# Performance work log

Hardware: AMD Instinct MI355X
Metric: run time of the kernel (lower is better)

## Reference

```python
import jax, jax.numpy as jnp
import numpy as np

H = 256       # hidden_dim
DICT = 30     # dict_size
SOS = 1       # symb2int['<sos>']

def gru_cell(x, h, Wih, Whh, bih, bhh):
    # PyTorch GRU cell math
    gi = x @ Wih.T + bih
    gh = h @ Whh.T + bhh
    ir, iz, inn = jnp.split(gi, 3, axis=-1)
    hr, hz, hn = jnp.split(gh, 3, axis=-1)
    r = jax.nn.sigmoid(ir + hr)
    z = jax.nn.sigmoid(iz + hz)
    n = jnp.tanh(inn + r * hn)
    return (1.0 - z) * n + z * h

def run_gru(xs, h0, Wih, Whh, bih, bhh):
    # xs: [T, B, F] -> outputs [T, B, Hc], final hidden [B, Hc]
    def step(h, x):
        h = gru_cell(x, h, Wih, Whh, bih, bhh)
        return h, h
    hT, out = jax.lax.scan(step, h0, xs)
    return out, hT

def setup_inputs() -> dict:
    key = jax.random.key(0)
    ks = jax.random.split(key, 24)
    B, T, L = 128, 512, 64
    se = 1.0 / np.sqrt(H)        # encoder GRU init scale
    sd = 1.0 / np.sqrt(2 * H)    # decoder GRU / linears scale
    def r(k, shape, sc):
        return jax.random.normal(k, shape, jnp.float32) * sc
    return {
        "x": jax.random.normal(ks[0], (B, T, 2), jnp.float32),
        "target_seq": jax.random.randint(ks[1], (B, L), 0, DICT),
        # encoder GRU, forward direction
        "enc_Wih_f": r(ks[2], (3 * H, 2), se), "enc_Whh_f": r(ks[3], (3 * H, H), se),
        "enc_bih_f": r(ks[4], (3 * H,), se),   "enc_bhh_f": r(ks[5], (3 * H,), se),
        # encoder GRU, backward direction
        "enc_Wih_b": r(ks[6], (3 * H, 2), se), "enc_Whh_b": r(ks[7], (3 * H, H), se),
        "enc_bih_b": r(ks[8], (3 * H,), se),   "enc_bhh_b": r(ks[9], (3 * H,), se),
        # decoder embedding + GRU (hidden 2H)
        "emb": r(ks[10], (DICT, H), 1.0),
        "dec_Wih": r(ks[11], (6 * H, H), sd),     "dec_Whh": r(ks[12], (6 * H, 2 * H), sd),
        "dec_bih": r(ks[13], (6 * H,), sd),       "dec_bhh": r(ks[14], (6 * H,), sd),
        # hidden2query, att_combine, fc
        "Wq": r(ks[15], (2 * H, 2 * H), sd), "bq": r(ks[16], (2 * H,), sd),
        "Wc": r(ks[17], (H, 4 * H), sd),     "bc": r(ks[18], (H,), sd),
        "Wf": r(ks[19], (DICT, H), se),      "bf": r(ks[20], (DICT,), se),
    }

def reference(x, target_seq,
              enc_Wih_f, enc_Whh_f, enc_bih_f, enc_bhh_f,
              enc_Wih_b, enc_Whh_b, enc_bih_b, enc_bhh_b,
              emb, dec_Wih, dec_Whh, dec_bih, dec_bhh,
              Wq, bq, Wc, bc, Wf, bf):
    B = x.shape[0]
    xs = jnp.transpose(x, (1, 0, 2))                # [T, B, 2]
    h0 = jnp.zeros((B, H), x.dtype)
    out_f, hf = run_gru(xs, h0, enc_Wih_f, enc_Whh_f, enc_bih_f, enc_bhh_f)
    out_b, hb = run_gru(xs[::-1], h0, enc_Wih_b, enc_Whh_b, enc_bih_b, enc_bhh_b)
    enc_out = jnp.concatenate([out_f, out_b[::-1]], axis=-1)  # [T, B, 2H]
    enc_out = jnp.transpose(enc_out, (1, 0, 2))               # [B, T, 2H]
    hidden = jnp.concatenate([hf, hb], axis=-1)               # [B, 2H]

    # teacher-forced decoder inputs: <sos>, target[0], ..., target[L-2]
    sos = jnp.full((B, 1), SOS, target_seq.dtype)
    toks = jnp.concatenate([sos, target_seq[:, :-1]], axis=1).T  # [L, B]

    def dec_step(h, tok):
        e = emb[tok]                                           # [B, H]
        h = gru_cell(e, h, dec_Wih, dec_Whh, dec_bih, dec_bhh) # [B, 2H]
        q = h @ Wq.T + bq                                      # hidden2query
        w = jax.nn.softmax(jnp.einsum('bh,bth->bt', q, enc_out), axis=-1)
        ctx = jnp.einsum('bt,bth->bh', w, enc_out)             # [B, 2H]
        o = jnp.concatenate([h, ctx], axis=-1) @ Wc.T + bc     # att_combine
        logits = o @ Wf.T + bf                                 # fc
        return h, (logits, w)

    hT, (logits, ws) = jax.lax.scan(dec_step, hidden, toks)
    vec_out = jnp.transpose(logits, (1, 0, 2))   # [B, L, DICT]
    attn = jnp.transpose(ws, (1, 2, 0))          # [B, T, L]
    return vec_out, hT[None], attn
```

## Files before the change

kernel.cpp:

```cpp
#include <hip/hip_runtime.h>
#include <hip/hip_bf16.h>

typedef unsigned int u32;
typedef unsigned short u16;
typedef _Float16 f16;
typedef f16 f16x2 __attribute__((ext_vector_type(2)));

#define BB 128
#define TT 512
#define HE 256
#define G3E 768
#define HD 512
#define G3D 1536
#define LL 64
#define NDICT 30
#define EMBD 256

__device__ __forceinline__ float fexp2(float v){
#if __has_builtin(__builtin_amdgcn_exp2f)
  return __builtin_amdgcn_exp2f(v);
#else
  return exp2f(v);
#endif
}
__device__ __forceinline__ float frcp(float v){
#if __has_builtin(__builtin_amdgcn_rcpf)
  return __builtin_amdgcn_rcpf(v);
#else
  return 1.f/v;
#endif
}
__device__ __forceinline__ float sigm(float v){
  return frcp(1.f + fexp2(-1.4426950408889634f*v));
}
__device__ __forceinline__ float ftanh(float v){
  float e = fexp2(fminf(v, 40.f)*2.8853901631790583f);
  return (e - 1.f)*frcp(e + 1.f);
}
__device__ __forceinline__ u16 f2h(float f){ return __builtin_bit_cast(u16, (f16)f); }
__device__ __forceinline__ float h2f(u16 b){ return (float)__builtin_bit_cast(f16, b); }
__device__ __forceinline__ u32 pkh2(float a, float b){
  u16 lo = __builtin_bit_cast(u16, (f16)a);
  u16 hi = __builtin_bit_cast(u16, (f16)b);
  return (u32)lo | ((u32)hi << 16);
}
__device__ __forceinline__ u32 pkrtz(float a, float b){
  return __builtin_bit_cast(u32, __builtin_amdgcn_cvt_pkrtz(a, b));
}
__device__ __forceinline__ f16x2 bc2(u32 v){ return __builtin_bit_cast(f16x2, v); }

__device__ __forceinline__ ushort4 hpk4(float a, float b, float c, float d){
  ushort4 r; r.x=f2h(a); r.y=f2h(b); r.z=f2h(c); r.w=f2h(d); return r;
}

__device__ __forceinline__ float dot2h(u32 a, u32 b, float acc){
#if __has_builtin(__builtin_amdgcn_fdot2)
  return __builtin_amdgcn_fdot2(bc2(a), bc2(b), acc, false);
#else
  float d;
  asm("v_dot2_f32_f16 %0, %1, %2, %3" : "=v"(d) : "v"(a), "v"(b), "v"(acc));
  return d;
#endif
}
__device__ __forceinline__ void dot_u4(uint4 wv, uint4 hv, float& acc){
  acc = dot2h(wv.x, hv.x, acc);
  acc = dot2h(wv.y, hv.y, acc);
  acc = dot2h(wv.z, hv.z, acc);
  acc = dot2h(wv.w, hv.w, acc);
}

#define INNER8P(Q0,Q1)                                                  \
  _Pragma("unroll")                                                     \
  for (int kp = 0; kp < 16; ++kp){                                      \
    uint4 a2 = *(const uint4*)&A2_s[kp*68 + (Q0)*4];                    \
    uint4 b2 = *(const uint4*)&B2_s[kp*68 + (Q1)*4];                    \
    acc[0] =dot2h(a2.x,b2.x,acc[0]);  acc[1] =dot2h(a2.x,b2.y,acc[1]);  \
    acc[2] =dot2h(a2.x,b2.z,acc[2]);  acc[3] =dot2h(a2.x,b2.w,acc[3]);  \
    acc[4] =dot2h(a2.y,b2.x,acc[4]);  acc[5] =dot2h(a2.y,b2.y,acc[5]);  \
    acc[6] =dot2h(a2.y,b2.z,acc[6]);  acc[7] =dot2h(a2.y,b2.w,acc[7]);  \
    acc[8] =dot2h(a2.z,b2.x,acc[8]);  acc[9] =dot2h(a2.z,b2.y,acc[9]);  \
    acc[10]=dot2h(a2.z,b2.z,acc[10]); acc[11]=dot2h(a2.z,b2.w,acc[11]); \
    acc[12]=dot2h(a2.w,b2.x,acc[12]); acc[13]=dot2h(a2.w,b2.y,acc[13]); \
    acc[14]=dot2h(a2.w,b2.z,acc[14]); acc[15]=dot2h(a2.w,b2.w,acc[15]); \
  }

__global__ __launch_bounds__(256) void k_prep_pairT(const float* __restrict__ src,
                                                    u32* __restrict__ dst, int N, int K){
  int idx = blockIdx.x*256 + threadIdx.x;
  int KP = K >> 1;
  if (idx < N*KP){
    int n = idx / KP, kp = idx - n*KP;
    dst[(size_t)kp*N + n] = pkh2(src[(size_t)n*K + 2*kp], src[(size_t)n*K + 2*kp + 1]);
  }
}

__global__ __launch_bounds__(256) void k_prep_wenc(const float* __restrict__ WF,
                                                   const float* __restrict__ WB,
                                                   uint4* __restrict__ dst){
  int idx = blockIdx.x*256 + threadIdx.x;
  int dir = idx / 24576, rem = idx - dir*24576;
  int i = rem >> 9, t = rem & 511;
  int rg = t >> 3, cg = t & 7;
  int k = i >> 2, q = i & 3;
  const float* s = (dir ? WB : WF) + (size_t)(rg*12 + k)*HE + cg*32 + q*8;
  uint4 v; v.x=pkh2(s[0],s[1]); v.y=pkh2(s[2],s[3]); v.z=pkh2(s[4],s[5]); v.w=pkh2(s[6],s[7]);
  dst[idx] = v;
}

__global__ __launch_bounds__(256) void k_prep_wdec(const float* __restrict__ src,
                                                   uint4* __restrict__ dst){
  int idx = blockIdx.x*256 + threadIdx.x;
  int lane = idx & 63;
  int ci = lane & 7, kq = lane >> 3;
  int rest = idx >> 6;
  int u = rest & 7, g = (rest >> 3) % 3, cg = rest / 24;
  int row = g*512 + cg*8 + ci;
  int col = kq*64 + u*8;
  const float* s = src + (size_t)row*HD + col;
  uint4 v; v.x=pkh2(s[0],s[1]); v.y=pkh2(s[2],s[3]); v.z=pkh2(s[4],s[5]); v.w=pkh2(s[6],s[7]);
  dst[idx] = v;
}

__global__ __launch_bounds__(256) void k_gi_tab(const float* __restrict__ emb,
                                                const float* __restrict__ Wih,
                                                const float* __restrict__ bih,
                                                float* __restrict__ gi){
  int v = blockIdx.x, gy = blockIdx.y;
  int g = gy*256 + threadIdx.x;
  __shared__ float e_s[EMBD];
  if (threadIdx.x < EMBD) e_s[threadIdx.x] = emb[(size_t)v*EMBD + threadIdx.x];
  __syncthreads();
  const float4* w4 = (const float4*)(Wih + (size_t)g*EMBD);
  float acc = 0.f;
  #pragma unroll 8
  for (int k = 0; k < EMBD/4; ++k){
    float4 w = w4[k];
    float4 h = *(const float4*)&e_s[k*4];
    acc = fmaf(w.x,h.x,fmaf(w.y,h.y,fmaf(w.z,h.z,fmaf(w.w,h.w,acc))));
  }
  gi[(size_t)v*G3D + g] = acc + bih[g];
}

__global__ __launch_bounds__(256) void k_h0cvt(const float* __restrict__ src,
                                               f16* __restrict__ dst){
  int i = blockIdx.x*256 + threadIdx.x;
  dst[i] = (f16)src[i];
}

__global__ __launch_bounds__(512, 2) void k_enc_p(
    const float* __restrict__ x,
    const uint4* __restrict__ Wp,
    const float* __restrict__ WihF, const float* __restrict__ WihB,
    const float* __restrict__ bihF, const float* __restrict__ bhhF,
    const float* __restrict__ bihB, const float* __restrict__ bhhB,
    u16* __restrict__ enc_out, float* __restrict__ h0out)
{
  const int b   = blockIdx.x >> 1;
  const int dir = blockIdx.x & 1;
  const int tid = threadIdx.x;
  const int cg  = tid & 7;
  const float* Wih = dir ? WihB : WihF;
  const float* bih = dir ? bihB : bihF;
  const float* bhh = dir ? bhhB : bhhF;

  __shared__ __align__(16) f16 h_pad[8*40];
  __shared__ float p_lds[G3E*9];

  uint4 w4[48];
  {
    const uint4* wsrc = Wp + (size_t)dir*24576 + tid;
    #pragma unroll
    for (int i = 0; i < 48; ++i) w4[i] = wsrc[(size_t)i*512];
  }
  float wv0r=0.f,wv1r=0.f,wv0z=0.f,wv1z=0.f,wv0n=0.f,wv1n=0.f;
  float br=0.f,bz=0.f,bin=0.f,bhn=0.f;
  float h_own = 0.f;
  if (tid < HE){
    const int j = tid;
    wv0r = Wih[j*2];         wv1r = Wih[j*2+1];
    wv0z = Wih[(j+HE)*2];    wv1z = Wih[(j+HE)*2+1];
    wv0n = Wih[(j+2*HE)*2];  wv1n = Wih[(j+2*HE)*2+1];
    br  = bih[j] + bhh[j];
    bz  = bih[j+HE] + bhh[j+HE];
    bin = bih[j+2*HE];
    bhn = bhh[j+2*HE];
    h_pad[(j >> 5)*40 + (j & 31)] = (f16)0.f;
  }
  const int rowbase = (tid >> 3)*12;
  __syncthreads();

  for (int t = 0; t < TT; ++t){
    const int tt = dir ? (TT-1-t) : t;
    const float x0 = x[((size_t)b*TT + tt)*2 + 0];
    const float x1 = x[((size_t)b*TT + tt)*2 + 1];

    {
      const uint4* hv = (const uint4*)(h_pad + cg*40);
      uint4 h0 = hv[0], h1 = hv[1], h2 = hv[2], h3 = hv[3];
      #pragma unroll
      for (int k = 0; k < 12; ++k){
        float a = 0.f;
        dot_u4(w4[k*4+0], h0, a);
        dot_u4(w4[k*4+1], h1, a);
        dot_u4(w4[k*4+2], h2, a);
        dot_u4(w4[k*4+3], h3, a);
        p_lds[(rowbase + k)*9 + cg] = a;
      }
    }
    __syncthreads();
    if (tid < HE){
      const int j = tid;
      float sr=0.f, sz=0.f, sn=0.f;
      #pragma unroll
      for (int k = 0; k < 8; ++k){
        sr += p_lds[j*9 + k];
        sz += p_lds[(j+HE)*9 + k];
        sn += p_lds[(j+2*HE)*9 + k];
      }
      float gr = sr + fmaf(wv0r, x0, wv1r*x1) + br;
      float gz = sz + fmaf(wv0z, x0, wv1z*x1) + bz;
      float gni = fmaf(wv0n, x0, wv1n*x1) + bin;
      float r = sigm(gr), z = sigm(gz);
      float n = ftanh(gni + r*(sn + bhn));
      float hnew = (1.f - z)*n + z*h_own;
      h_own = hnew;
      h_pad[(j >> 5)*40 + (j & 31)] = (f16)hnew;
      enc_out[((size_t)b*TT + tt)*HD + dir*HE + j] = f2h(hnew);
    }
    __syncthreads();
  }
  if (tid < HE) h0out[(size_t)b*HD + dir*HE + tid] = h_own;
}

__global__ __launch_bounds__(256, 2) void k_dstep(
    const int* __restrict__ tgt, const float* __restrict__ gi_tab,
    const uint4* __restrict__ Wd2, const float* __restrict__ bhh,
    const f16* __restrict__ h_prev, f16* __restrict__ h_next,
    float* __restrict__ Hall, int l)
{
  const int bg = blockIdx.x & 7, cg = blockIdx.x >> 3;
  const int tid = threadIdx.x;
  const int ci = tid & 7, kq = (tid >> 3) & 7, bq = tid >> 6;

  __shared__ __align__(16) f16 h_s[16][8][72];
  __shared__ float p_s[3][16][8][9];
  __shared__ int tok_s[16];

  uint4 w[24];
  {
    const uint4* wp = Wd2 + (size_t)cg*24*64 + (kq*8 + ci);
    #pragma unroll
    for (int i = 0; i < 24; ++i) w[i] = wp[(size_t)i*64];
  }
  {
    const uint4* hsrc = (const uint4*)(h_prev + (size_t)bg*16*HD);
    #pragma unroll
    for (int i = 0; i < 4; ++i){
      int idx = tid + i*256;
      int b = idx >> 6, w4 = idx & 63;
      int kq2 = w4 >> 3, off = w4 & 7;
      *(uint4*)&h_s[b][kq2][off*8] = hsrc[idx];
    }
  }
  if (tid < 16) tok_s[tid] = (l == 0) ? 1 : tgt[(size_t)(bg*16 + tid)*LL + l - 1];
  __syncthreads();

  #pragma unroll
  for (int nb = 0; nb < 4; ++nb){
    const int b = bq*4 + nb;
    const uint4* hv = (const uint4*)&h_s[b][kq][0];
    float x0 = 0.f, x1 = 0.f, x2 = 0.f;
    #pragma unroll
    for (int u = 0; u < 8; ++u){
      uint4 hh = hv[u];
      dot_u4(w[u],      hh, x0);
      dot_u4(w[8 + u],  hh, x1);
      dot_u4(w[16 + u], hh, x2);
    }
    p_s[0][b][ci][kq] = x0;
    p_s[1][b][ci][kq] = x1;
    p_s[2][b][ci][kq] = x2;
  }
  __syncthreads();

  if (tid < 128){
    const int b = tid >> 3, cl = tid & 7;
    const int C = cg*8 + cl;
    float s0 = 0.f, s1 = 0.f, s2 = 0.f;
    #pragma unroll
    for (int k = 0; k < 8; ++k){
      s0 += p_s[0][b][cl][k];
      s1 += p_s[1][b][cl][k];
      s2 += p_s[2][b][cl][k];
    }
    const int tok = tok_s[b];
    const float* gp = gi_tab + (size_t)tok*G3D + C;
    float r = sigm(gp[0]    + s0 + bhh[C]);
    float z = sigm(gp[HD]   + s1 + bhh[HD + C]);
    float n = ftanh(gp[2*HD] + r*(s2 + bhh[2*HD + C]));
    float hp = (float)h_s[b][C >> 6][C & 63];
    float hnew = (1.f - z)*n + z*hp;
    const int gb = bg*16 + b;
    h_next[(size_t)gb*HD + C] = (f16)hnew;
    Hall[((size_t)l*BB + gb)*HD + C] = hnew;
  }
}

__global__ __launch_bounds__(256) void k_query(const float* __restrict__ Hall,
                                               const u32* __restrict__ Wq2,
                                               const float* __restrict__ bq,
                                               u16* __restrict__ Qh){
  const int rt = blockIdx.x, nt = blockIdx.y;
  const int tid = threadIdx.x;
  __shared__ u32 A2_s[16*68];
  __shared__ u32 B2_s[16*68];
  const int rq = tid >> 4, nq = tid & 15;
  const int i = tid >> 2, jj = tid & 3;
  const int i3 = tid >> 4, n4 = tid & 15;
  float acc[16] = {};
  for (int kc = 0; kc < 16; ++kc){
    __syncthreads();
    {
      const float* src = Hall + (size_t)(rt*64 + i)*HD + kc*32 + jj*8;
      float4 v0 = *(const float4*)src, v1 = *(const float4*)(src+4);
      A2_s[(jj*4+0)*68+i] = pkrtz(v0.x, v0.y);
      A2_s[(jj*4+1)*68+i] = pkrtz(v0.z, v0.w);
      A2_s[(jj*4+2)*68+i] = pkrtz(v1.x, v1.y);
      A2_s[(jj*4+3)*68+i] = pkrtz(v1.z, v1.w);
    }
    {
      uint4 v = *(const uint4*)(Wq2 + (size_t)(kc*16 + i3)*HD + nt*64 + n4*4);
      *(uint4*)&B2_s[i3*68 + n4*4] = v;
    }
    __syncthreads();
    INNER8P(rq, nq)
  }
  const int n0 = nt*64 + nq*4;
  float4 bv = *(const float4*)&bq[n0];
  #pragma unroll
  for (int r = 0; r < 4; ++r){
    u16* dst = Qh + (size_t)(rt*64 + rq*4 + r)*HD + n0;
    *(ushort4*)dst = hpk4(acc[r*4+0]+bv.x, acc[r*4+1]+bv.y,
                          acc[r*4+2]+bv.z, acc[r*4+3]+bv.w);
  }
}

__global__ __launch_bounds__(256) void k_scores(const u16* __restrict__ Qh,
                                                const u16* __restrict__ enc,
                                                float* __restrict__ Sbuf){
  const int bI = blockIdx.x, tt = blockIdx.y;
  const int tid = threadIdx.x;
  __shared__ u32 A2_s[16*68];
  __shared__ u32 B2_s[16*68];
  const int lq = tid >> 4, tq = tid & 15;
  const int i = tid >> 2, jj = tid & 3;
  float acc[16] = {};
  for (int kc = 0; kc < 16; ++kc){
    __syncthreads();
    {
      uint4 va = *(const uint4*)(Qh + ((size_t)i*BB + bI)*HD + kc*32 + jj*8);
      A2_s[(jj*4+0)*68+i] = va.x;
      A2_s[(jj*4+1)*68+i] = va.y;
      A2_s[(jj*4+2)*68+i] = va.z;
      A2_s[(jj*4+3)*68+i] = va.w;
    }
    {
      uint4 vb = *(const uint4*)(enc + ((size_t)bI*TT + tt*64 + i)*HD + kc*32 + jj*8);
      B2_s[(jj*4+0)*68+i] = vb.x;
      B2_s[(jj*4+1)*68+i] = vb.y;
      B2_s[(jj*4+2)*68+i] = vb.z;
      B2_s[(jj*4+3)*68+i] = vb.w;
    }
    __syncthreads();
    INNER8P(lq, tq)
  }
  #pragma unroll
  for (int r = 0; r < 4; ++r){
    float4 o = make_float4(acc[r*4+0],acc[r*4+1],acc[r*4+2],acc[r*4+3]);
    *(float4*)&Sbuf[((size_t)bI*LL + lq*4+r)*TT + tt*64 + tq*4] = o;
  }
}

__global__ __launch_bounds__(64) void k_softmax(const float* __restrict__ Sbuf,
                                                u16* __restrict__ Ph){
  const int row = blockIdx.x;
  const int lane = threadIdx.x;
  const float* s = Sbuf + (size_t)row*TT;
  float v[8]; float m = -1e30f;
  #pragma unroll
  for (int i = 0; i < 8; ++i){ v[i] = s[lane + i*64]; m = fmaxf(m, v[i]); }
  #pragma unroll
  for (int o = 32; o; o >>= 1) m = fmaxf(m, __shfl_xor(m, o));
  float Z = 0.f;
  #pragma unroll
  for (int i = 0; i < 8; ++i){ v[i] = fexp2(1.4426950408889634f*(v[i] - m)); Z += v[i]; }
  #pragma unroll
  for (int o = 32; o; o >>= 1) Z += __shfl_xor(Z, o);
  float inv = frcp(Z);
  u16* p = Ph + (size_t)row*TT;
  #pragma unroll
  for (int i = 0; i < 8; ++i) p[lane + i*64] = f2h(v[i]*inv);
}

__global__ __launch_bounds__(256) void k_attn_tr(const u16* __restrict__ Ph,
                                                 float* __restrict__ att){
  const int bI = blockIdx.x, tt = blockIdx.y;
  const int tid = threadIdx.x;
  __shared__ u16 tile[64][72];
  {
    const int i = tid >> 2, jj = tid & 3;
    #pragma unroll
    for (int rep = 0; rep < 2; ++rep){
      int ch = jj + rep*4;
      uint4 v = *(const uint4*)(Ph + ((size_t)bI*LL + i)*TT + tt*64 + ch*8);
      *(uint4*)&tile[i][ch*8] = v;
    }
  }
  __syncthreads();
  const int t = tid >> 2, jl = tid & 3;
  #pragma unroll
  for (int rep = 0; rep < 4; ++rep){
    int l0 = jl*16 + rep*4;
    float4 o;
    o.x = h2f(tile[l0+0][t]); o.y = h2f(tile[l0+1][t]);
    o.z = h2f(tile[l0+2][t]); o.w = h2f(tile[l0+3][t]);
    *(float4*)&att[((size_t)bI*TT + tt*64 + t)*LL + l0] = o;
  }
}

__global__ __launch_bounds__(256) void k_ctx(const u16* __restrict__ Ph,
                                             const u16* __restrict__ enc,
                                             u16* __restrict__ ctxh){
  const int bI = blockIdx.x, nt = blockIdx.y;
  const int tid = threadIdx.x;
  __shared__ u32 A2_s[16*68];
  __shared__ u32 B2_s[16*68];
  const int lq = tid >> 4, nq = tid & 15;
  const int i = tid >> 2, jj = tid & 3;
  const int q = tid >> 4, n4 = tid & 15;
  float acc[16] = {};
  for (int tc = 0; tc < 16; ++tc){
    __syncthreads();
    {
      uint4 va = *(const uint4*)(Ph + ((size_t)bI*LL + i)*TT + tc*32 + jj*8);
      A2_s[(jj*4+0)*68+i] = va.x;
      A2_s[(jj*4+1)*68+i] = va.y;
      A2_s[(jj*4+2)*68+i] = va.z;
      A2_s[(jj*4+3)*68+i] = va.w;
    }
    {
      const int t0 = tc*32 + 2*q;
      const int n0 = nt*64 + n4*4;
      uint2 a = *(const uint2*)(enc + ((size_t)bI*TT + t0)*HD + n0);
      uint2 b = *(const uint2*)(enc + ((size_t)bI*TT + t0 + 1)*HD + n0);
      B2_s[q*68 + n4*4 + 0] = (a.x & 0xffffu) | (b.x << 16);
      B2_s[q*68 + n4*4 + 1] = (a.x >> 16) | (b.x & 0xffff0000u);
      B2_s[q*68 + n4*4 + 2] = (a.y & 0xffffu) | (b.y << 16);
      B2_s[q*68 + n4*4 + 3] = (a.y >> 16) | (b.y & 0xffff0000u);
    }
    __syncthreads();
    INNER8P(lq, nq)
  }
  const int n0 = nt*64 + nq*4;
  #pragma unroll
  for (int r = 0; r < 4; ++r){
    int ll = lq*4 + r;
    u16* dst = ctxh + ((size_t)ll*BB + bI)*HD + n0;
    *(ushort4*)dst = hpk4(acc[r*4+0], acc[r*4+1], acc[r*4+2], acc[r*4+3]);
  }
}

__global__ __launch_bounds__(256) void k_outc(const float* __restrict__ Hall,
                                              const u16* __restrict__ ctxh,
                                              const u32* __restrict__ Wc2,
                                              const float* __restrict__ bc,
                                              float* __restrict__ obuf){
  const int rt = blockIdx.x, nt = blockIdx.y;
  const int tid = threadIdx.x;
  __shared__ u32 A2_s[16*68];
  __shared__ u32 B2_s[16*68];
  const int rq = tid >> 4, nq = tid & 15;
  const int i = tid >> 2, jj = tid & 3;
  const int i3 = tid >> 4, n4 = tid & 15;
  float acc[16] = {};
  for (int kc = 0; kc < 32; ++kc){
    __syncthreads();
    if (kc < 16){
      const float* src = Hall + (size_t)(rt*64 + i)*HD + kc*32 + jj*8;
      float4 v0 = *(const float4*)src, v1 = *(const float4*)(src+4);
      A2_s[(jj*4+0)*68+i] = pkrtz(v0.x, v0.y);
      A2_s[(jj*4+1)*68+i] = pkrtz(v0.z, v0.w);
      A2_s[(jj*4+2)*68+i] = pkrtz(v1.x, v1.y);
      A2_s[(jj*4+3)*68+i] = pkrtz(v1.z, v1.w);
    } else {
      uint4 v = *(const uint4*)(ctxh + (size_t)(rt*64 + i)*HD + (kc-16)*32 + jj*8);
      A2_s[(jj*4+0)*68+i] = v.x;
      A2_s[(jj*4+1)*68+i] = v.y;
      A2_s[(jj*4+2)*68+i] = v.z;
      A2_s[(jj*4+3)*68+i] = v.w;
    }
    {
      uint4 v = *(const uint4*)(Wc2 + (size_t)(kc*16 + i3)*256 + nt*64 + n4*4);
      *(uint4*)&B2_s[i3*68 + n4*4] = v;
    }
    __syncthreads();
    INNER8P(rq, nq)
  }
  const int n0 = nt*64 + nq*4;
  float4 bv = *(const float4*)&bc[n0];
  #pragma unroll
  for (int r = 0; r < 4; ++r){
    float4 o = make_float4(acc[r*4+0]+bv.x, acc[r*4+1]+bv.y,
                           acc[r*4+2]+bv.z, acc[r*4+3]+bv.w);
    *(float4*)&obuf[(size_t)(rt*64 + rq*4 + r)*256 + n0] = o;
  }
}

__global__ __launch_bounds__(256) void k_fc(const float* __restrict__ obuf,
                                            const float* __restrict__ Wf,
                                            const float* __restrict__ bfv,
                                            float* __restrict__ out_vec){
  const int rt = blockIdx.x;
  const int tid = threadIdx.x;
  __shared__ float w_s[30*260];
  for (int rr = 0; rr < 30; ++rr) w_s[rr*260 + tid] = Wf[(size_t)rr*256 + tid];
  __syncthreads();
  const int rl = tid >> 2, dq = tid & 3;
  const int r = rt*64 + rl;
  float acc[8] = {};
  for (int k = 0; k < 256; k += 4){
    float4 o4 = *(const float4*)&obuf[(size_t)r*256 + k];
    #pragma unroll
    for (int jq = 0; jq < 8; ++jq){
      int d = dq*8 + jq;
      if (d < 30){
        float4 w4 = *(const float4*)&w_s[d*260 + k];
        acc[jq] = fmaf(o4.x,w4.x,fmaf(o4.y,w4.y,fmaf(o4.z,w4.z,fmaf(o4.w,w4.w,acc[jq]))));
      }
    }
  }
  const int b = r & 127, l = r >> 7;
  #pragma unroll
  for (int jq = 0; jq < 8; ++jq){
    int d = dq*8 + jq;
    if (d < 30) out_vec[((size_t)b*LL + l)*NDICT + d] = acc[jq] + bfv[d];
  }
}

__global__ __launch_bounds__(256) void k_copy(const float* __restrict__ src,
                                              float* __restrict__ dst, int n){
  int i = blockIdx.x*256 + threadIdx.x;
  if (i < n) dst[i] = src[i];
}

extern "C" void kernel_launch(void* const* d_in, const int* in_sizes, int n_in,
                              void* d_out, int out_size, void* d_ws, size_t ws_size,
                              hipStream_t stream)
{
  const float* x     = (const float*)d_in[0];
  const int*   tgt   = (const int*)  d_in[1];
  const float* eWihF = (const float*)d_in[2];
  const float* eWhhF = (const float*)d_in[3];
  const float* ebihF = (const float*)d_in[4];
  const float* ebhhF = (const float*)d_in[5];
  const float* eWihB = (const float*)d_in[6];
  const float* eWhhB = (const float*)d_in[7];
  const float* ebihB = (const float*)d_in[8];
  const float* ebhhB = (const float*)d_in[9];
  const float* emb   = (const float*)d_in[10];
  const float* dWih  = (const float*)d_in[11];
  const float* dWhh  = (const float*)d_in[12];
  const float* dbih  = (const float*)d_in[13];
  const float* dbhh  = (const float*)d_in[14];
  const float* Wq    = (const float*)d_in[15];
  const float* bq    = (const float*)d_in[16];
  const float* Wc    = (const float*)d_in[17];
  const float* bc    = (const float*)d_in[18];
  const float* Wf    = (const float*)d_in[19];
  const float* bfv   = (const float*)d_in[20];

  char* w = (char*)d_ws;
  uint4* Wpenc = (uint4*)w; w += 786432;
  uint4* Wpdec = (uint4*)w; w += 1572864;
  u32*   Wq2   = (u32*)w;  w += 524288;
  u32*   Wc2   = (u32*)w;  w += 524288;
  float* gi_t  = (float*)w; w += 184320;
  float* h0buf = (float*)w; w += 262144;
  f16*   h16A  = (f16*)w; w += 131072;
  f16*   h16B  = (f16*)w; w += 131072;
  float* Hall  = (float*)w; w += 16777216;
  u16*   Qh    = (u16*)w;
  u16*   Ph    = (u16*)w; w += 8388608;
  float* Sbuf  = (float*)w;
  u16*   ctxh  = (u16*)w; w += 8388608;
  float* obuf  = (float*)w; w += 8388608;
  u16*   ench  = (u16*)w; w += 67108864;

  float* out     = (float*)d_out;
  float* out_vec = out;
  float* out_hT  = out + (size_t)BB*LL*NDICT;
  float* out_att = out_hT + (size_t)BB*HD;

  k_prep_wenc<<<192, 256, 0, stream>>>(eWhhF, eWhhB, Wpenc);
  k_prep_wdec<<<384, 256, 0, stream>>>(dWhh, Wpdec);
  k_prep_pairT<<<512, 256, 0, stream>>>(Wq, Wq2, HD, HD);
  k_prep_pairT<<<512, 256, 0, stream>>>(Wc, Wc2, 256, 1024);
  k_gi_tab<<<dim3(NDICT, 6), 256, 0, stream>>>(emb, dWih, dbih, gi_t);

  k_enc_p<<<BB*2, 512, 0, stream>>>(x, Wpenc, eWihF, eWihB,
                                    ebihF, ebhhF, ebihB, ebhhB, ench, h0buf);

  k_h0cvt<<<256, 256, 0, stream>>>(h0buf, h16A);
  for (int l = 0; l < LL; ++l){
    const f16* hp = (l & 1) ? h16B : h16A;
    f16*       hn = (l & 1) ? h16A : h16B;
    k_dstep<<<512, 256, 0, stream>>>(tgt, gi_t, Wpdec, dbhh, hp, hn, Hall, l);
  }

  k_query<<<dim3(128,8), 256, 0, stream>>>(Hall, Wq2, bq, Qh);
  k_scores<<<dim3(128,8), 256, 0, stream>>>(Qh, ench, Sbuf);
  k_softmax<<<BB*LL, 64, 0, stream>>>(Sbuf, Ph);
  k_attn_tr<<<dim3(128,8), 256, 0, stream>>>(Ph, out_att);
  k_ctx<<<dim3(128,8), 256, 0, stream>>>(Ph, ench, ctxh);
  k_outc<<<dim3(128,4), 256, 0, stream>>>(Hall, ctxh, Wc2, bc, obuf);
  k_fc<<<BB, 256, 0, stream>>>(obuf, Wf, bfv, out_vec);
  k_copy<<<(BB*HD+255)/256, 256, 0, stream>>>(Hall + (size_t)63*BB*HD, out_hT, BB*HD);
}
```

Baseline: 1.164 ms.

## Rewrite encoder GRU recurrence with MFMA batching 16 sequences per block

New measurement: 2.605 ms. 124% more time.

```diff
diff --git a/kernel.cpp b/kernel.cpp
--- a/kernel.cpp
+++ b/kernel.cpp
@@ -5,6 +5,8 @@
 typedef unsigned short u16;
 typedef _Float16 f16;
 typedef f16 f16x2 __attribute__((ext_vector_type(2)));
+typedef f16 f16x4v __attribute__((ext_vector_type(4)));
+typedef float f32x4v __attribute__((ext_vector_type(4)));
 
 #define BB 128
 #define TT 512
@@ -51,6 +53,21 @@
 
 __device__ __forceinline__ ushort4 hpk4(float a, float b, float c, float d){
   ushort4 r; r.x=f2h(a); r.y=f2h(b); r.z=f2h(c); r.w=f2h(d); return r;
+}
+
+__device__ __forceinline__ f32x4v mfma16(uint2 a, uint2 b, f32x4v c){
+#if __has_builtin(__builtin_amdgcn_mfma_f32_16x16x16f16)
+  return __builtin_amdgcn_mfma_f32_16x16x16f16(
+      __builtin_bit_cast(f16x4v, a), __builtin_bit_cast(f16x4v, b), c, 0, 0, 0);
+#elif __has_builtin(__builtin_amdgcn_mfma_f32_16x16x16_f16)
+  return __builtin_amdgcn_mfma_f32_16x16x16_f16(
+      __builtin_bit_cast(f16x4v, a), __builtin_bit_cast(f16x4v, b), c, 0, 0, 0);
+#else
+  f32x4v d;
+  asm("v_mfma_f32_16x16x16_f16 %0, %1, %2, %3"
+      : "=v"(d) : "v"(a), "v"(b), "v"(c));
+  return d;
+#endif
 }
 
 __device__ __forceinline__ float dot2h(u32 a, u32 b, float acc){
@@ -94,17 +111,54 @@
   }
 }
 
-__global__ __launch_bounds__(256) void k_prep_wenc(const float* __restrict__ WF,
-                                                   const float* __restrict__ WB,
-                                                   uint4* __restrict__ dst){
+__global__ __launch_bounds__(256) void k_prep_aH(const float* __restrict__ WF,
+                                                 const float* __restrict__ WB,
+                                                 uint2* __restrict__ dst){
   int idx = blockIdx.x*256 + threadIdx.x;
-  int dir = idx / 24576, rem = idx - dir*24576;
-  int i = rem >> 9, t = rem & 511;
-  int rg = t >> 3, cg = t & 7;
-  int k = i >> 2, q = i & 3;
-  const float* s = (dir ? WB : WF) + (size_t)(rg*12 + k)*HE + cg*32 + q*8;
-  uint4 v; v.x=pkh2(s[0],s[1]); v.y=pkh2(s[2],s[3]); v.z=pkh2(s[4],s[5]); v.w=pkh2(s[6],s[7]);
+  int l = idx & 63;
+  int s = (idx >> 6) & 15;
+  int rem = idx >> 10;
+  int t6 = rem % 6, wd = rem / 6;
+  int w = wd & 7, dir = wd >> 3;
+  int g = t6 >> 1, q = t6 & 1;
+  int row = g*256 + w*32 + q*16 + (l & 15);
+  int k0 = s*16 + (l >> 4)*4;
+  const float* W = (dir ? WB : WF) + (size_t)row*HE + k0;
+  uint2 v; v.x = pkh2(W[0], W[1]); v.y = pkh2(W[2], W[3]);
   dst[idx] = v;
+}
+
+__global__ __launch_bounds__(256) void k_prep_aX(const float* __restrict__ WihF,
+                                                 const float* __restrict__ WihB,
+                                                 const float* __restrict__ bihF,
+                                                 const float* __restrict__ bhhF,
+                                                 const float* __restrict__ bihB,
+                                                 const float* __restrict__ bhhB,
+                                                 uint2* __restrict__ dst){
+  int idx = blockIdx.x*256 + threadIdx.x;
+  if (idx >= 6144) return;
+  int l = idx & 63;
+  int rem = idx >> 6;
+  int t6 = rem % 6, wd = rem / 6;
+  int w = wd & 7, dir = wd >> 3;
+  int g = t6 >> 1, q = t6 & 1;
+  int row = g*256 + w*32 + q*16 + (l & 15);
+  int kx0 = (l >> 4)*4;
+  const float* Wih = dir ? WihB : WihF;
+  const float* bih = dir ? bihB : bihF;
+  const float* bhh = dir ? bhhB : bhhF;
+  float v[4];
+  #pragma unroll
+  for (int e = 0; e < 4; ++e){
+    int kx = kx0 + e;
+    float val = 0.f;
+    if (kx == 0) val = Wih[row*2];
+    else if (kx == 1) val = Wih[row*2 + 1];
+    else if (kx == 2) val = bih[row] + (row < 512 ? bhh[row] : 0.f);
+    v[e] = val;
+  }
+  uint2 o; o.x = pkh2(v[0], v[1]); o.y = pkh2(v[2], v[3]);
+  dst[idx] = o;
 }
 
 __global__ __launch_bounds__(256) void k_prep_wdec(const float* __restrict__ src,
@@ -147,89 +201,126 @@
   dst[i] = (f16)src[i];
 }
 
-__global__ __launch_bounds__(512, 2) void k_enc_p(
+__global__ __launch_bounds__(512, 1) void k_enc_m(
     const float* __restrict__ x,
-    const uint4* __restrict__ Wp,
-    const float* __restrict__ WihF, const float* __restrict__ WihB,
-    const float* __restrict__ bihF, const float* __restrict__ bhhF,
-    const float* __restrict__ bihB, const float* __restrict__ bhhB,
+    const uint2* __restrict__ AH, const uint2* __restrict__ AX,
+    const float* __restrict__ bhhF, const float* __restrict__ bhhB,
     u16* __restrict__ enc_out, float* __restrict__ h0out)
 {
-  const int b   = blockIdx.x >> 1;
-  const int dir = blockIdx.x & 1;
-  const int tid = threadIdx.x;
-  const int cg  = tid & 7;
-  const float* Wih = dir ? WihB : WihF;
-  const float* bih = dir ? bihB : bihF;
+  const int dir = blockIdx.x & 1, bg = blockIdx.x >> 1;
+  const int tid = threadIdx.x, w = tid >> 6, l = tid & 63;
+  const int col = l & 15, kg = l >> 4;
   const float* bhh = dir ? bhhB : bhhF;
 
-  __shared__ __align__(16) f16 h_pad[8*40];
-  __shared__ float p_lds[G3E*9];
-
-  uint4 w4[48];
+  __shared__ __align__(16) uint2 Hb[2][16][64];
+  __shared__ __align__(16) uint2 AXl[48][64];
+  __shared__ float2 x_s[2][16];
+
+  uint2 aH[6][16];
   {
-    const uint4* wsrc = Wp + (size_t)dir*24576 + tid;
-    #pragma unroll
-    for (int i = 0; i < 48; ++i) w4[i] = wsrc[(size_t)i*512];
-  }
-  float wv0r=0.f,wv1r=0.f,wv0z=0.f,wv1z=0.f,wv0n=0.f,wv1n=0.f;
-  float br=0.f,bz=0.f,bin=0.f,bhn=0.f;
-  float h_own = 0.f;
-  if (tid < HE){
-    const int j = tid;
-    wv0r = Wih[j*2];         wv1r = Wih[j*2+1];
-    wv0z = Wih[(j+HE)*2];    wv1z = Wih[(j+HE)*2+1];
-    wv0n = Wih[(j+2*HE)*2];  wv1n = Wih[(j+2*HE)*2+1];
-    br  = bih[j] + bhh[j];
-    bz  = bih[j+HE] + bhh[j+HE];
-    bin = bih[j+2*HE];
-    bhn = bhh[j+2*HE];
-    h_pad[(j >> 5)*40 + (j & 31)] = (f16)0.f;
-  }
-  const int rowbase = (tid >> 3)*12;
+    const uint2* src = AH + ((size_t)(dir*8 + w)*6)*16*64 + l;
+    #pragma unroll
+    for (int t6 = 0; t6 < 6; ++t6)
+      #pragma unroll
+      for (int s = 0; s < 16; ++s)
+        aH[t6][s] = src[(size_t)(t6*16 + s)*64];
+  }
+  {
+    const uint2* src = AX + ((size_t)(dir*8 + w)*6)*64 + l;
+    #pragma unroll
+    for (int t6 = 0; t6 < 6; ++t6) AXl[w*6 + t6][l] = src[(size_t)t6*64];
+  }
+  f32x4v bhn0, bhn1;
+  #pragma unroll
+  for (int r = 0; r < 4; ++r){
+    bhn0[r] = bhh[2*HE + w*32 +      kg*4 + r];
+    bhn1[r] = bhh[2*HE + w*32 + 16 + kg*4 + r];
+  }
+  {
+    int i0 = tid*2;
+    Hb[0][i0 >> 6][i0 & 63] = make_uint2(0u, 0u);
+    Hb[0][(i0+1) >> 6][(i0+1) & 63] = make_uint2(0u, 0u);
+  }
+  if (tid < 16){
+    int tt0 = dir ? (TT-1) : 0;
+    x_s[0][tid] = *(const float2*)&x[((size_t)(bg*16 + tid)*TT + tt0)*2];
+  }
   __syncthreads();
 
+  int cur = 0;
   for (int t = 0; t < TT; ++t){
     const int tt = dir ? (TT-1-t) : t;
-    const float x0 = x[((size_t)b*TT + tt)*2 + 0];
-    const float x1 = x[((size_t)b*TT + tt)*2 + 1];
-
-    {
-      const uint4* hv = (const uint4*)(h_pad + cg*40);
-      uint4 h0 = hv[0], h1 = hv[1], h2 = hv[2], h3 = hv[3];
+    uint2 b[16];
+    #pragma unroll
+    for (int s = 0; s < 16; ++s) b[s] = Hb[cur][s][l];
+    float2 xv = x_s[t & 1][col];
+    uint2 b16;
+    if (kg == 0){ b16.x = pkh2(xv.x, xv.y); b16.y = pkh2(1.f, 0.f); }
+    else { b16.x = 0u; b16.y = 0u; }
+    uint2 aXf[6];
+    #pragma unroll
+    for (int t6 = 0; t6 < 6; ++t6) aXf[t6] = AXl[w*6 + t6][l];
+
+    f32x4v accR0 = {0,0,0,0}, accR1 = {0,0,0,0};
+    f32x4v accZ0 = {0,0,0,0}, accZ1 = {0,0,0,0};
+    f32x4v accN0 = bhn0, accN1 = bhn1;
+    #pragma unroll
+    for (int s = 0; s < 16; ++s){
+      accR0 = mfma16(aH[0][s], b[s], accR0);
+      accR1 = mfma16(aH[1][s], b[s], accR1);
+      accZ0 = mfma16(aH[2][s], b[s], accZ0);
+      accZ1 = mfma16(aH[3][s], b[s], accZ1);
+      accN0 = mfma16(aH[4][s], b[s], accN0);
+      accN1 = mfma16(aH[5][s], b[s], accN1);
+    }
+    accR0 = mfma16(aXf[0], b16, accR0);
+    accR1 = mfma16(aXf[1], b16, accR1);
+    accZ0 = mfma16(aXf[2], b16, accZ0);
+    accZ1 = mfma16(aXf[3], b16, accZ1);
+    f32x4v z4 = {0,0,0,0};
+    f32x4v gin0 = mfma16(aXf[4], b16, z4);
+    f32x4v gin1 = mfma16(aXf[5], b16, z4);
+
+    #pragma unroll
+    for (int q = 0; q < 2; ++q){
+      f32x4v aR = q ? accR1 : accR0;
+      f32x4v aZ = q ? accZ1 : accZ0;
+      f32x4v aN = q ? accN1 : accN0;
+      f32x4v aG = q ? gin1 : gin0;
+      uint2 hOld = b[w*2 + q];
+      f16x2 plo = bc2(hOld.x), phi = bc2(hOld.y);
+      float ho[4] = {(float)plo.x, (float)plo.y, (float)phi.x, (float)phi.y};
+      float hn[4];
       #pragma unroll
-      for (int k = 0; k < 12; ++k){
-        float a = 0.f;
-        dot_u4(w4[k*4+0], h0, a);
-        dot_u4(w4[k*4+1], h1, a);
-        dot_u4(w4[k*4+2], h2, a);
-        dot_u4(w4[k*4+3], h3, a);
-        p_lds[(rowbase + k)*9 + cg] = a;
+      for (int r = 0; r < 4; ++r){
+        float R = sigm(aR[r]);
+        float Z = sigm(aZ[r]);
+        float N = ftanh(aG[r] + R*aN[r]);
+        hn[r] = (1.f - Z)*N + Z*ho[r];
       }
-    }
-    __syncthreads();
-    if (tid < HE){
-      const int j = tid;
-      float sr=0.f, sz=0.f, sn=0.f;
-      #pragma unroll
-      for (int k = 0; k < 8; ++k){
-        sr += p_lds[j*9 + k];
-        sz += p_lds[(j+HE)*9 + k];
-        sn += p_lds[(j+2*HE)*9 + k];
-      }
-      float gr = sr + fmaf(wv0r, x0, wv1r*x1) + br;
-      float gz = sz + fmaf(wv0z, x0, wv1z*x1) + bz;
-      float gni = fmaf(wv0n, x0, wv1n*x1) + bin;
-      float r = sigm(gr), z = sigm(gz);
-      float n = ftanh(gni + r*(sn + bhn));
-      float hnew = (1.f - z)*n + z*h_own;
-      h_own = hnew;
-      h_pad[(j >> 5)*40 + (j & 31)] = (f16)hnew;
-      enc_out[((size_t)b*TT + tt)*HD + dir*HE + j] = f2h(hnew);
-    }
-    __syncthreads();
-  }
-  if (tid < HE) h0out[(size_t)b*HD + dir*HE + tid] = h_own;
+      const int j0 = w*32 + q*16 + kg*4;
+      *(ushort4*)&enc_out[((size_t)(bg*16 + col)*TT + tt)*HD + dir*HE + j0]
+          = hpk4(hn[0], hn[1], hn[2], hn[3]);
+      uint2 hw; hw.x = pkh2(hn[0], hn[1]); hw.y = pkh2(hn[2], hn[3]);
+      Hb[cur ^ 1][w*2 + q][l] = hw;
+    }
+    if (tid < 16 && t + 1 < TT){
+      int tt1 = dir ? (TT-2-t) : (t+1);
+      x_s[(t+1) & 1][tid] = *(const float2*)&x[((size_t)(bg*16 + tid)*TT + tt1)*2];
+    }
+    __syncthreads();
+    cur ^= 1;
+  }
+  #pragma unroll
+  for (int q = 0; q < 2; ++q){
+    uint2 hv = Hb[cur][w*2 + q][l];
+    f16x2 plo = bc2(hv.x), phi = bc2(hv.y);
+    float ho[4] = {(float)plo.x, (float)plo.y, (float)phi.x, (float)phi.y};
+    const int j0 = w*32 + q*16 + kg*4;
+    #pragma unroll
+    for (int r = 0; r < 4; ++r)
+      h0out[(size_t)(bg*16 + col)*HD + dir*HE + j0 + r] = ho[r];
+  }
 }
 
 __global__ __launch_bounds__(256, 2) void k_dstep(
@@ -580,7 +671,8 @@
   const float* bfv   = (const float*)d_in[20];
 
   char* w = (char*)d_ws;
-  uint4* Wpenc = (uint4*)w; w += 786432;
+  uint2* AHp   = (uint2*)w; w += 786432;
+  uint2* AXp   = (uint2*)w; w += 49152;
   uint4* Wpdec = (uint4*)w; w += 1572864;
   u32*   Wq2   = (u32*)w;  w += 524288;
   u32*   Wc2   = (u32*)w;  w += 524288;
@@ -601,14 +693,14 @@
   float* out_hT  = out + (size_t)BB*LL*NDICT;
   float* out_att = out_hT + (size_t)BB*HD;
 
-  k_prep_wenc<<<192, 256, 0, stream>>>(eWhhF, eWhhB, Wpenc);
+  k_prep_aH<<<384, 256, 0, stream>>>(eWhhF, eWhhB, AHp);
+  k_prep_aX<<<24, 256, 0, stream>>>(eWihF, eWihB, ebihF, ebhhF, ebihB, ebhhB, AXp);
   k_prep_wdec<<<384, 256, 0, stream>>>(dWhh, Wpdec);
   k_prep_pairT<<<512, 256, 0, stream>>>(Wq, Wq2, HD, HD);
   k_prep_pairT<<<512, 256, 0, stream>>>(Wc, Wc2, 256, 1024);
   k_gi_tab<<<dim3(NDICT, 6), 256, 0, stream>>>(emb, dWih, dbih, gi_t);
 
-  k_enc_p<<<BB*2, 512, 0, stream>>>(x, Wpenc, eWihF, eWihB,
-                                    ebihF, ebhhF, ebihB, ebhhB, ench, h0buf);
+  k_enc_m<<<16, 512, 0, stream>>>(x, AHp, AXp, ebhhF, ebhhB, ench, h0buf);
 
   k_h0cvt<<<256, 256, 0, stream>>>(h0buf, h16A);
   for (int l = 0; l < LL; ++l){
```
